# Kernel tuning notes

Hardware: AMD Instinct MI355X
Metric: run time of the kernel (lower is better)

The kernel has to match this reference:

```python
import jax, jax.numpy as jnp
import numpy as np

B, N = 4, 2048
P = N * (N - 1) // 2  # number of upper-triangular pairs
CUTOFF = 5.0
BOX_SCALE = 20.0  # spread points so the 5.0 cutoff gives a sparse graph


def setup_inputs() -> dict:
    key = jax.random.key(0)
    x = jax.random.normal(key, (B, N, 3), dtype=jnp.float32) * BOX_SCALE
    return {"x": x}


def reference(x):
    b, n = x.shape[0], x.shape[1]
    p = n * (n - 1) // 2
    rows, cols = jnp.triu_indices(n, k=1)          # each [P]
    idx0 = jnp.stack([rows, cols], axis=0)          # [2, P]
    # pairwise difference via gather (matches index_select + view in torch)
    diff = x[:, rows, :] - x[:, cols, :]            # [B, P, 3]
    dist = jnp.sqrt(jnp.sum(diff * diff, axis=-1))  # [B, P]
    mask = (dist <= CUTOFF).ravel()                 # [B*P]
    # compaction: valid flat indices first, padded with -1 (jit-static size)
    flat_idx = jnp.nonzero(mask, size=b * p, fill_value=-1)[0]  # [B*P]
    valid = flat_idx >= 0
    safe = jnp.where(valid, flat_idx, 0)
    idx1 = safe // p                                # batch index of each edge
    idx2 = safe % p                                 # pair index of each edge
    out = idx0[:, idx2] + idx1[None, :] * n         # [2, B*P]
    out = jnp.where(valid[None, :], out, -1)        # pad invalid edges with -1
    return out.astype(jnp.int64)
```

## Files before the change

kernel.cpp:

```cpp
#include <hip/hip_runtime.h>
#include <stdint.h>


namespace {
constexpr int kB = 4;
constexpr int kN = 2048;
constexpr int kP = kN * (kN - 1) / 2;
constexpr long long kTotal = (long long)kB * kP;
constexpr float kCut2 = 25.0f;
constexpr int kCap = 128;
constexpr int kNCBlk = 4096;
constexpr int kTile = 256;
constexpr int kNT = kN / kTile;
constexpr int kTPairs = kNT * (kNT + 1) / 2;
constexpr int kJS = 4;
constexpr int kSliceJ = kTile / kJS;
constexpr int kNF = kB * kTPairs * kJS;
constexpr int kFillBlk = 2048;
constexpr int kGrid1 = kNF + kFillBlk;
constexpr int kFillN4 = (int)(2 * kTotal / 4);
constexpr int kFillPerBlk = 2048;
}

__device__ __forceinline__ void decode_pair(int p, int& i, int& j) {
  float t = sqrtf((float)(16769025 - 8 * p));
  int ii = (int)((4095.0f - t) * 0.5f);
  ii = ii < 0 ? 0 : (ii > kN - 2 ? kN - 2 : ii);
  while (ii > 0 && (ii * (4095 - ii)) / 2 > p) --ii;
  while (ii < kN - 2 && ((ii + 1) * (4094 - ii)) / 2 <= p) ++ii;
  i = ii;
  j = ii + 1 + (p - (ii * (4095 - ii)) / 2);
}

__device__ __forceinline__ bool pair_test(const float* __restrict__ x, int b, int p,
                                          int& gi, int& gj) {
  int i, j;
  decode_pair(p, i, j);
  const float* xb = x + (size_t)b * kN * 3;
  float dx = xb[3 * i + 0] - xb[3 * j + 0];
  float dy = xb[3 * i + 1] - xb[3 * j + 1];
  float dz = xb[3 * i + 2] - xb[3 * j + 2];
  gi = b * kN + i;
  gj = b * kN + j;
  return dx * dx + dy * dy + dz * dz <= kCut2;
}

__global__ __launch_bounds__(256) void fill_find_kernel(
    const float* __restrict__ x, uint32_t* __restrict__ counts,
    int2* __restrict__ stash, int* __restrict__ out) {
  const int t = threadIdx.x;
  const int bid = blockIdx.x;

  if (bid >= kNF) {
    const int4 m1 = make_int4(-1, -1, -1, -1);
    int4* o = (int4*)out;
    const int base = (bid - kNF) * kFillPerBlk;
#pragma unroll
    for (int s = 0; s < 8; ++s) {
      const int idx = base + s * 256 + t;
      if (idx < kFillN4) o[idx] = m1;
    }
    return;
  }

  __shared__ float4 sp[kSliceJ];

  const int b = bid / (kTPairs * kJS);
  const int rem = bid - b * (kTPairs * kJS);
  const int u = rem / kJS;
  const int js = rem - u * kJS;
  int ti = 0, rowlen = kNT, acc = 0;
  while (acc + rowlen <= u) { acc += rowlen; --rowlen; ++ti; }
  const int tj = ti + (u - acc);

  const float3* __restrict__ xb3 = (const float3*)(x + (size_t)b * kN * 3);
  const int jbase = tj * kTile + js * kSliceJ;
  if (t < kSliceJ) {
    const float3 pj = xb3[jbase + t];
    sp[t] = make_float4(pj.x, pj.y, pj.z, 0.0f);
  }
  const int i = ti * kTile + t;
  const float3 pi = xb3[i];
  __syncthreads();

  const int gib = b << 11;
  const uint32_t Ci = (uint32_t)((i * (4095 - i)) >> 1);
  const int cbb = b << 10;
  const bool diag = (ti == tj);
  const int jrel0 = js * kSliceJ;

  auto emit = [&](uint32_t m, int jb0) {
    do {
      const int k = __ffs(m) - 1;
      m &= m - 1;
      const int j = jbase + jb0 + k;
      const uint32_t pf = Ci + (uint32_t)(j - i - 1);
      const int cb = cbb + (int)(pf >> 11);
      const uint32_t slot = atomicAdd(&counts[cb], 1u);
      if (slot < (uint32_t)kCap)
        stash[(size_t)cb * kCap + slot] = make_int2(gib + i, gib + j);
    } while (m);
  };

#pragma unroll
  for (int jb = 0; jb < kSliceJ; jb += 8) {
    uint32_t m = 0;
#pragma unroll
    for (int k = 0; k < 8; ++k) {
      const float4 c = sp[jb + k];
      const float dx = pi.x - c.x;
      const float dy = pi.y - c.y;
      const float dz = pi.z - c.z;
      const bool hit = (dx * dx + dy * dy + dz * dz <= kCut2) &&
                       (!diag || (jrel0 + jb + k) > t);
      m |= (uint32_t)hit << k;
    }
    if (m) emit(m, jb);
  }
}

__global__ __launch_bounds__(256) void scatter_kernel(
    const float* __restrict__ x, const uint32_t* __restrict__ counts,
    const int2* __restrict__ stash, int* __restrict__ out) {
  const int bid = blockIdx.x;
  const int t = threadIdx.x;

  const uint32_t cnt = counts[bid];
  if (cnt == 0) return;

  const uint4* c4 = (const uint4*)counts;
  uint32_t part = 0;
#pragma unroll
  for (int q = 0; q < 4; ++q) {
    uint4 v = c4[t * 4 + q];
    int i0 = t * 16 + q * 4;
    part += (i0 + 0 < bid) ? v.x : 0u;
    part += (i0 + 1 < bid) ? v.y : 0u;
    part += (i0 + 2 < bid) ? v.z : 0u;
    part += (i0 + 3 < bid) ? v.w : 0u;
  }
  for (int o = 32; o > 0; o >>= 1) part += __shfl_down(part, o, 64);
  __shared__ uint32_t wred[4];
  if ((t & 63) == 0) wred[t >> 6] = part;
  __syncthreads();
  if (t == 0) wred[0] = wred[0] + wred[1] + wred[2] + wred[3];
  __syncthreads();
  const uint32_t off = wred[0];

  if (cnt <= (uint32_t)kCap) {
    __shared__ int2 ebuf[kCap];
    __shared__ uint32_t pfb[kCap];
    for (uint32_t e = t; e < cnt; e += 256) {
      int2 v = stash[(size_t)bid * kCap + e];
      ebuf[e] = v;
      int i = v.x & 2047, j = v.y & 2047;
      pfb[e] = (uint32_t)((i * (4095 - i)) / 2 + (j - i - 1));
    }
    __syncthreads();
    for (uint32_t e = t; e < cnt; e += 256) {
      uint32_t mypf = pfb[e];
      uint32_t rank = 0;
      for (uint32_t f = 0; f < cnt; ++f) rank += (pfb[f] < mypf) ? 1u : 0u;
      out[off + rank] = ebuf[e].x;
      out[(size_t)kTotal + off + rank] = ebuf[e].y;
    }
    return;
  }

  const int wave = t >> 6, lane = t & 63;
  const int b = bid >> 10;
  const int p0 = (bid & 1023) << 11;
  __shared__ uint32_t slot[32];
  unsigned long long masks[8];
  int gi[8], gj[8];
  bool fl[8];
#pragma unroll
  for (int k = 0; k < 8; ++k) {
    int p = p0 + k * 256 + t;
    fl[k] = (p < kP) && pair_test(x, b, p, gi[k], gj[k]);
    masks[k] = __ballot(fl[k]);
    if (lane == 0) slot[k * 4 + wave] = (uint32_t)__popcll(masks[k]);
  }
  __syncthreads();
  if (t == 0) {
    uint32_t run = 0;
    for (int s = 0; s < 32; ++s) {
      uint32_t c = slot[s];
      slot[s] = run;
      run += c;
    }
  }
  __syncthreads();
#pragma unroll
  for (int k = 0; k < 8; ++k) {
    if (fl[k]) {
      uint32_t pos = off + slot[k * 4 + wave] +
                     (uint32_t)__popcll(masks[k] & ((1ULL << lane) - 1ULL));
      out[pos] = gi[k];
      out[(size_t)kTotal + pos] = gj[k];
    }
  }
}

extern "C" void kernel_launch(void* const* d_in, const int* in_sizes, int n_in,
                              void* d_out, int out_size, void* d_ws, size_t ws_size,
                              hipStream_t stream) {
  const float* x = (const float*)d_in[0];
  int* out = (int*)d_out;
  uint32_t* counts = (uint32_t*)d_ws;
  int2* stash = (int2*)(counts + 4096);

  (void)hipMemsetAsync(counts, 0, kNCBlk * sizeof(uint32_t), stream);
  hipLaunchKernelGGL(fill_find_kernel, dim3(kGrid1), dim3(256), 0, stream, x,
                     counts, stash, out);
  hipLaunchKernelGGL(scatter_kernel, dim3(kNCBlk), dim3(256), 0, stream, x, counts,
                     stash, out);
}
```

Baseline: 31.67 us.

## Move -1 padding fill into output-chunk compose kernel, skipping rewrite of written slots

The -1 fill of the whole output no longer runs as extra blocks inside the find kernel. A second kernel now owns output chunks, and each chunk block writes both the edges and the padding. Blocks whose chunk lies past the total edge count only write -1, while chunks holding edges scan the prefix offsets and write any edges that fall inside their span. The goal is to stop writing -1 into slots that later get edge values, removing double writes and the store-ordering dependency. The cost is serial per-thread rank and recompute loops in the few edge-holding chunks, which could be slow if edges concentrate in a few blocks.

```diff
diff --git a/kernel.cpp b/kernel.cpp
--- a/kernel.cpp
+++ b/kernel.cpp
@@ -16,10 +16,8 @@
 constexpr int kJS = 4;
 constexpr int kSliceJ = kTile / kJS;
 constexpr int kNF = kB * kTPairs * kJS;
-constexpr int kFillBlk = 2048;
-constexpr int kGrid1 = kNF + kFillBlk;
-constexpr int kFillN4 = (int)(2 * kTotal / 4);
-constexpr int kFillPerBlk = 2048;
+constexpr int kChunk = 4096;
+constexpr int kGrid2 = (int)(kTotal / kChunk);
 }
 
 __device__ __forceinline__ void decode_pair(int p, int& i, int& j) {
@@ -45,25 +43,14 @@
   return dx * dx + dy * dy + dz * dz <= kCut2;
 }
 
-__global__ __launch_bounds__(256) void fill_find_kernel(
+__global__ __launch_bounds__(256) void find_kernel(
     const float* __restrict__ x, uint32_t* __restrict__ counts,
-    int2* __restrict__ stash, int* __restrict__ out) {
+    uint32_t* __restrict__ total, int2* __restrict__ stash) {
   const int t = threadIdx.x;
   const int bid = blockIdx.x;
 
-  if (bid >= kNF) {
-    const int4 m1 = make_int4(-1, -1, -1, -1);
-    int4* o = (int4*)out;
-    const int base = (bid - kNF) * kFillPerBlk;
-#pragma unroll
-    for (int s = 0; s < 8; ++s) {
-      const int idx = base + s * 256 + t;
-      if (idx < kFillN4) o[idx] = m1;
-    }
-    return;
-  }
-
   __shared__ float4 sp[kSliceJ];
+  __shared__ uint32_t blkEdges;
 
   const int b = bid / (kTPairs * kJS);
   const int rem = bid - b * (kTPairs * kJS);
@@ -79,6 +66,7 @@
     const float3 pj = xb3[jbase + t];
     sp[t] = make_float4(pj.x, pj.y, pj.z, 0.0f);
   }
+  if (t == 0) blkEdges = 0;
   const int i = ti * kTile + t;
   const float3 pi = xb3[i];
   __syncthreads();
@@ -99,6 +87,7 @@
       const uint32_t slot = atomicAdd(&counts[cb], 1u);
       if (slot < (uint32_t)kCap)
         stash[(size_t)cb * kCap + slot] = make_int2(gib + i, gib + j);
+      atomicAdd(&blkEdges, 1u);
     } while (m);
   };
 
@@ -117,87 +106,132 @@
     }
     if (m) emit(m, jb);
   }
-}
-
-__global__ __launch_bounds__(256) void scatter_kernel(
+
+  __syncthreads();
+  if (t == 0 && blkEdges) atomicAdd(&total[bid & 7], blkEdges);
+}
+
+__global__ __launch_bounds__(256) void fill_compose_kernel(
     const float* __restrict__ x, const uint32_t* __restrict__ counts,
-    const int2* __restrict__ stash, int* __restrict__ out) {
+    const uint32_t* __restrict__ total, const int2* __restrict__ stash,
+    int* __restrict__ out) {
+  const int t = threadIdx.x;
+  const int wave = t >> 6, lane = t & 63;
   const int bid = blockIdx.x;
-  const int t = threadIdx.x;
-
-  const uint32_t cnt = counts[bid];
-  if (cnt == 0) return;
-
-  const uint4* c4 = (const uint4*)counts;
-  uint32_t part = 0;
-#pragma unroll
-  for (int q = 0; q < 4; ++q) {
-    uint4 v = c4[t * 4 + q];
-    int i0 = t * 16 + q * 4;
-    part += (i0 + 0 < bid) ? v.x : 0u;
-    part += (i0 + 1 < bid) ? v.y : 0u;
-    part += (i0 + 2 < bid) ? v.z : 0u;
-    part += (i0 + 3 < bid) ? v.w : 0u;
-  }
-  for (int o = 32; o > 0; o >>= 1) part += __shfl_down(part, o, 64);
+  const int base = bid * kChunk;
+
+  uint32_t T;
+  {
+    const uint4* t4 = (const uint4*)total;
+    uint4 a = t4[0], bb = t4[1];
+    T = a.x + a.y + a.z + a.w + bb.x + bb.y + bb.z + bb.w;
+  }
+
+  int4* o0 = (int4*)out + (base >> 2);
+  int4* o1 = (int4*)(out + kTotal) + (base >> 2);
+
+  if ((uint32_t)base >= T) {
+    const int4 m1 = make_int4(-1, -1, -1, -1);
+#pragma unroll
+    for (int s = 0; s < 4; ++s) {
+      o0[t + s * 256] = m1;
+      o1[t + s * 256] = m1;
+    }
+    return;
+  }
+
+  __shared__ uint32_t offs[kNCBlk];
   __shared__ uint32_t wred[4];
-  if ((t & 63) == 0) wred[t >> 6] = part;
+  {
+    uint32_t c[16];
+    const uint4* c4 = (const uint4*)counts;
+    uint32_t tsum = 0;
+#pragma unroll
+    for (int q = 0; q < 4; ++q) {
+      uint4 v = c4[t * 4 + q];
+      c[q * 4 + 0] = v.x; c[q * 4 + 1] = v.y;
+      c[q * 4 + 2] = v.z; c[q * 4 + 3] = v.w;
+      tsum += v.x + v.y + v.z + v.w;
+    }
+    uint32_t run = tsum;
+    for (int o = 1; o < 64; o <<= 1) {
+      uint32_t u = __shfl_up(run, o, 64);
+      if (lane >= o) run += u;
+    }
+    if (lane == 63) wred[wave] = run;
+    __syncthreads();
+    uint32_t wb = 0;
+    for (int w = 0; w < 4; ++w)
+      if (w < wave) wb += wred[w];
+    uint32_t excl = wb + run - tsum;
+#pragma unroll
+    for (int q = 0; q < 16; ++q) {
+      offs[t * 16 + q] = excl;
+      excl += c[q];
+    }
+  }
   __syncthreads();
-  if (t == 0) wred[0] = wred[0] + wred[1] + wred[2] + wred[3];
-  __syncthreads();
-  const uint32_t off = wred[0];
-
-  if (cnt <= (uint32_t)kCap) {
-    __shared__ int2 ebuf[kCap];
-    __shared__ uint32_t pfb[kCap];
-    for (uint32_t e = t; e < cnt; e += 256) {
-      int2 v = stash[(size_t)bid * kCap + e];
-      ebuf[e] = v;
-      int i = v.x & 2047, j = v.y & 2047;
-      pfb[e] = (uint32_t)((i * (4095 - i)) / 2 + (j - i - 1));
-    }
-    __syncthreads();
-    for (uint32_t e = t; e < cnt; e += 256) {
-      uint32_t mypf = pfb[e];
-      uint32_t rank = 0;
-      for (uint32_t f = 0; f < cnt; ++f) rank += (pfb[f] < mypf) ? 1u : 0u;
-      out[off + rank] = ebuf[e].x;
-      out[(size_t)kTotal + off + rank] = ebuf[e].y;
-    }
-    return;
-  }
-
-  const int wave = t >> 6, lane = t & 63;
-  const int b = bid >> 10;
-  const int p0 = (bid & 1023) << 11;
-  __shared__ uint32_t slot[32];
-  unsigned long long masks[8];
-  int gi[8], gj[8];
-  bool fl[8];
-#pragma unroll
-  for (int k = 0; k < 8; ++k) {
-    int p = p0 + k * 256 + t;
-    fl[k] = (p < kP) && pair_test(x, b, p, gi[k], gj[k]);
-    masks[k] = __ballot(fl[k]);
-    if (lane == 0) slot[k * 4 + wave] = (uint32_t)__popcll(masks[k]);
-  }
-  __syncthreads();
-  if (t == 0) {
-    uint32_t run = 0;
-    for (int s = 0; s < 32; ++s) {
-      uint32_t c = slot[s];
-      slot[s] = run;
-      run += c;
-    }
-  }
-  __syncthreads();
-#pragma unroll
-  for (int k = 0; k < 8; ++k) {
-    if (fl[k]) {
-      uint32_t pos = off + slot[k * 4 + wave] +
-                     (uint32_t)__popcll(masks[k] & ((1ULL << lane) - 1ULL));
-      out[pos] = gi[k];
-      out[(size_t)kTotal + pos] = gj[k];
+
+  const uint32_t spanEnd = (uint32_t)base + (uint32_t)kChunk;
+
+  for (int cb = t; cb < kNCBlk; cb += 256) {
+    const uint32_t o = offs[cb];
+    if (o >= spanEnd) break;
+    const uint32_t cnt = counts[cb];
+    if (cnt == 0 || o + cnt <= (uint32_t)base) continue;
+
+    if (cnt <= (uint32_t)kCap) {
+      for (uint32_t f = 0; f < cnt; ++f) {
+        const int2 vf = stash[(size_t)cb * kCap + f];
+        const int fi = vf.x & 2047, fj = vf.y & 2047;
+        const uint32_t pff = (uint32_t)((fi * (4095 - fi)) / 2 + (fj - fi - 1));
+        uint32_t rank = 0;
+        for (uint32_t g = 0; g < cnt; ++g) {
+          const int2 vg = stash[(size_t)cb * kCap + g];
+          const int gi2 = vg.x & 2047, gj2 = vg.y & 2047;
+          const uint32_t pfg =
+              (uint32_t)((gi2 * (4095 - gi2)) / 2 + (gj2 - gi2 - 1));
+          rank += (pfg < pff) ? 1u : 0u;
+        }
+        const uint32_t pos = o + rank;
+        if (pos >= (uint32_t)base && pos < spanEnd) {
+          out[pos] = vf.x;
+          out[(size_t)kTotal + pos] = vf.y;
+        }
+      }
+    } else {
+      const int b_ = cb >> 10;
+      const int p0 = (cb & 1023) << 11;
+      uint32_t seen = 0;
+      for (int p = p0; p < p0 + 2048 && p < kP; ++p) {
+        int gi_, gj_;
+        if (pair_test(x, b_, p, gi_, gj_)) {
+          const uint32_t pos = o + seen;
+          if (pos >= (uint32_t)base && pos < spanEnd) {
+            out[pos] = gi_;
+            out[(size_t)kTotal + pos] = gj_;
+          }
+          ++seen;
+        }
+      }
+    }
+  }
+
+  {
+    const int4 m1 = make_int4(-1, -1, -1, -1);
+#pragma unroll
+    for (int r = 0; r < 2; ++r) {
+      int* __restrict__ row = out + (size_t)r * kTotal;
+#pragma unroll
+      for (int s = 0; s < 4; ++s) {
+        const int f = base + ((s * 256 + t) << 2);
+        if ((uint32_t)f >= T) {
+          *(int4*)(row + f) = m1;
+        } else if ((uint32_t)f + 4u > T) {
+          for (int e = 0; e < 4; ++e)
+            if ((uint32_t)(f + e) >= T) row[f + e] = -1;
+        }
+      }
     }
   }
 }
@@ -208,11 +242,12 @@
   const float* x = (const float*)d_in[0];
   int* out = (int*)d_out;
   uint32_t* counts = (uint32_t*)d_ws;
-  int2* stash = (int2*)(counts + 4096);
-
-  (void)hipMemsetAsync(counts, 0, kNCBlk * sizeof(uint32_t), stream);
-  hipLaunchKernelGGL(fill_find_kernel, dim3(kGrid1), dim3(256), 0, stream, x,
-                     counts, stash, out);
-  hipLaunchKernelGGL(scatter_kernel, dim3(kNCBlk), dim3(256), 0, stream, x, counts,
-                     stash, out);
-}
+  uint32_t* total = counts + kNCBlk;
+  int2* stash = (int2*)(counts + kNCBlk + 8);
+
+  (void)hipMemsetAsync(counts, 0, (kNCBlk + 8) * sizeof(uint32_t), stream);
+  hipLaunchKernelGGL(find_kernel, dim3(kNF), dim3(256), 0, stream, x, counts,
+                     total, stash);
+  hipLaunchKernelGGL(fill_compose_kernel, dim3(kGrid2), dim3(256), 0, stream, x,
+                     counts, total, stash, out);
+}
```

After: 116.9 us. +268.9%, slower.

## Move -1 padding fill into scatter kernel and skip the valid-edge prefix

Applied to the files above, without the earlier changes.

The -1 fill of the output moves out of the find kernel and into the scatter kernel, and now sets the row and column halves separately. To support this, the find kernel counts edges per block and accumulates a global edge total into eight atomic counters. The fill blocks read that total and write -1 only at positions at or beyond it. This avoids writing -1 over slots the scatter later overwrites and separates the find and fill work. In exchange it adds shared and global atomics to the find kernel. The large fill now shares a launch with scatter instead of overlapping the find phase.

```diff
diff --git a/kernel.cpp b/kernel.cpp
--- a/kernel.cpp
+++ b/kernel.cpp
@@ -7,6 +7,7 @@
 constexpr int kN = 2048;
 constexpr int kP = kN * (kN - 1) / 2;
 constexpr long long kTotal = (long long)kB * kP;
+constexpr int kTotInt = (int)kTotal;
 constexpr float kCut2 = 25.0f;
 constexpr int kCap = 128;
 constexpr int kNCBlk = 4096;
@@ -17,9 +18,7 @@
 constexpr int kSliceJ = kTile / kJS;
 constexpr int kNF = kB * kTPairs * kJS;
 constexpr int kFillBlk = 2048;
-constexpr int kGrid1 = kNF + kFillBlk;
-constexpr int kFillN4 = (int)(2 * kTotal / 4);
-constexpr int kFillPerBlk = 2048;
+constexpr int kGrid2 = kFillBlk + kNCBlk;
 }
 
 __device__ __forceinline__ void decode_pair(int p, int& i, int& j) {
@@ -45,25 +44,14 @@
   return dx * dx + dy * dy + dz * dz <= kCut2;
 }
 
-__global__ __launch_bounds__(256) void fill_find_kernel(
+__global__ __launch_bounds__(256) void find_kernel(
     const float* __restrict__ x, uint32_t* __restrict__ counts,
-    int2* __restrict__ stash, int* __restrict__ out) {
+    uint32_t* __restrict__ total, int2* __restrict__ stash) {
   const int t = threadIdx.x;
   const int bid = blockIdx.x;
 
-  if (bid >= kNF) {
-    const int4 m1 = make_int4(-1, -1, -1, -1);
-    int4* o = (int4*)out;
-    const int base = (bid - kNF) * kFillPerBlk;
-#pragma unroll
-    for (int s = 0; s < 8; ++s) {
-      const int idx = base + s * 256 + t;
-      if (idx < kFillN4) o[idx] = m1;
-    }
-    return;
-  }
-
   __shared__ float4 sp[kSliceJ];
+  __shared__ uint32_t blkEdges;
 
   const int b = bid / (kTPairs * kJS);
   const int rem = bid - b * (kTPairs * kJS);
@@ -79,6 +67,7 @@
     const float3 pj = xb3[jbase + t];
     sp[t] = make_float4(pj.x, pj.y, pj.z, 0.0f);
   }
+  if (t == 0) blkEdges = 0;
   const int i = ti * kTile + t;
   const float3 pi = xb3[i];
   __syncthreads();
@@ -90,9 +79,11 @@
   const int jrel0 = js * kSliceJ;
 
   auto emit = [&](uint32_t m, int jb0) {
+    uint32_t n = 0;
     do {
       const int k = __ffs(m) - 1;
       m &= m - 1;
+      ++n;
       const int j = jbase + jb0 + k;
       const uint32_t pf = Ci + (uint32_t)(j - i - 1);
       const int cb = cbb + (int)(pf >> 11);
@@ -100,6 +91,7 @@
       if (slot < (uint32_t)kCap)
         stash[(size_t)cb * kCap + slot] = make_int2(gib + i, gib + j);
     } while (m);
+    atomicAdd(&blkEdges, n);
   };
 
 #pragma unroll
@@ -117,15 +109,49 @@
     }
     if (m) emit(m, jb);
   }
-}
-
-__global__ __launch_bounds__(256) void scatter_kernel(
+
+  __syncthreads();
+  if (t == 0 && blkEdges) atomicAdd(&total[bid & 7], blkEdges);
+}
+
+__global__ __launch_bounds__(256) void fill_scatter_kernel(
     const float* __restrict__ x, const uint32_t* __restrict__ counts,
-    const int2* __restrict__ stash, int* __restrict__ out) {
+    const uint32_t* __restrict__ total, const int2* __restrict__ stash,
+    int* __restrict__ out) {
+  const int t = threadIdx.x;
   const int bid = blockIdx.x;
-  const int t = threadIdx.x;
-
-  const uint32_t cnt = counts[bid];
+
+  if (bid < kFillBlk) {
+    uint32_t T;
+    {
+      const uint4* t4 = (const uint4*)total;
+      const uint4 a = t4[0], b4 = t4[1];
+      T = a.x + a.y + a.z + a.w + b4.x + b4.y + b4.z + b4.w;
+    }
+    const int4 m1 = make_int4(-1, -1, -1, -1);
+    const int base = bid * 4096;
+#pragma unroll
+    for (int s = 0; s < 4; ++s) {
+      const int f = base + ((s * 256 + t) << 2);
+      if (f >= kTotInt) break;
+      if ((uint32_t)f >= T) {
+        *(int4*)(out + f) = m1;
+        *(int4*)(out + kTotal + f) = m1;
+      } else if ((uint32_t)f + 4u > T) {
+        for (int e = 0; e < 4; ++e) {
+          if ((uint32_t)(f + e) >= T) {
+            out[f + e] = -1;
+            out[kTotal + f + e] = -1;
+          }
+        }
+      }
+    }
+    return;
+  }
+
+  const int sbid = bid - kFillBlk;
+
+  const uint32_t cnt = counts[sbid];
   if (cnt == 0) return;
 
   const uint4* c4 = (const uint4*)counts;
@@ -134,10 +160,10 @@
   for (int q = 0; q < 4; ++q) {
     uint4 v = c4[t * 4 + q];
     int i0 = t * 16 + q * 4;
-    part += (i0 + 0 < bid) ? v.x : 0u;
-    part += (i0 + 1 < bid) ? v.y : 0u;
-    part += (i0 + 2 < bid) ? v.z : 0u;
-    part += (i0 + 3 < bid) ? v.w : 0u;
+    part += (i0 + 0 < sbid) ? v.x : 0u;
+    part += (i0 + 1 < sbid) ? v.y : 0u;
+    part += (i0 + 2 < sbid) ? v.z : 0u;
+    part += (i0 + 3 < sbid) ? v.w : 0u;
   }
   for (int o = 32; o > 0; o >>= 1) part += __shfl_down(part, o, 64);
   __shared__ uint32_t wred[4];
@@ -151,7 +177,7 @@
     __shared__ int2 ebuf[kCap];
     __shared__ uint32_t pfb[kCap];
     for (uint32_t e = t; e < cnt; e += 256) {
-      int2 v = stash[(size_t)bid * kCap + e];
+      int2 v = stash[(size_t)sbid * kCap + e];
       ebuf[e] = v;
       int i = v.x & 2047, j = v.y & 2047;
       pfb[e] = (uint32_t)((i * (4095 - i)) / 2 + (j - i - 1));
@@ -168,8 +194,8 @@
   }
 
   const int wave = t >> 6, lane = t & 63;
-  const int b = bid >> 10;
-  const int p0 = (bid & 1023) << 11;
+  const int b = sbid >> 10;
+  const int p0 = (sbid & 1023) << 11;
   __shared__ uint32_t slot[32];
   unsigned long long masks[8];
   int gi[8], gj[8];
@@ -208,11 +234,12 @@
   const float* x = (const float*)d_in[0];
   int* out = (int*)d_out;
   uint32_t* counts = (uint32_t*)d_ws;
-  int2* stash = (int2*)(counts + 4096);
-
-  (void)hipMemsetAsync(counts, 0, kNCBlk * sizeof(uint32_t), stream);
-  hipLaunchKernelGGL(fill_find_kernel, dim3(kGrid1), dim3(256), 0, stream, x,
-                     counts, stash, out);
-  hipLaunchKernelGGL(scatter_kernel, dim3(kNCBlk), dim3(256), 0, stream, x, counts,
-                     stash, out);
-}
+  uint32_t* total = counts + kNCBlk;
+  int2* stash = (int2*)(counts + kNCBlk + 8);
+
+  (void)hipMemsetAsync(counts, 0, (kNCBlk + 8) * sizeof(uint32_t), stream);
+  hipLaunchKernelGGL(find_kernel, dim3(kNF), dim3(256), 0, stream, x, counts,
+                     total, stash);
+  hipLaunchKernelGGL(fill_scatter_kernel, dim3(kGrid2), dim3(256), 0, stream, x,
+                     counts, total, stash, out);
+}
```

New measurement: 40.13 us. 1.27x slower.

## Replace global bucket stash with per-block LDS edge lists and global rank placement

Applied to the files above, without the earlier changes.

The find kernel now collects hits into a shared-memory list per tile block (LDS atomics) and writes them out with a per-block count. This replaces the global atomic counters and bucketed stash, which also removes the memset. A new place kernel gathers every block's hits into LDS, prefix-sums the counts, and ranks each edge against all edges to find its sorted output position. This removes global atomics and the fallback recompute path, but it makes every active block re-read all hit lists and adds a hard cap on the total edge count (kMaxT), which could give wrong output if that cap is exceeded.

```diff
diff --git a/kernel.cpp b/kernel.cpp
--- a/kernel.cpp
+++ b/kernel.cpp
@@ -8,8 +8,6 @@
 constexpr int kP = kN * (kN - 1) / 2;
 constexpr long long kTotal = (long long)kB * kP;
 constexpr float kCut2 = 25.0f;
-constexpr int kCap = 128;
-constexpr int kNCBlk = 4096;
 constexpr int kTile = 256;
 constexpr int kNT = kN / kTile;
 constexpr int kTPairs = kNT * (kNT + 1) / 2;
@@ -20,6 +18,8 @@
 constexpr int kGrid1 = kNF + kFillBlk;
 constexpr int kFillN4 = (int)(2 * kTotal / 4);
 constexpr int kFillPerBlk = 2048;
+constexpr int kCapF = 1024;
+constexpr int kMaxT = 14336;
 }
 
 __device__ __forceinline__ void decode_pair(int p, int& i, int& j) {
@@ -32,22 +32,9 @@
   j = ii + 1 + (p - (ii * (4095 - ii)) / 2);
 }
 
-__device__ __forceinline__ bool pair_test(const float* __restrict__ x, int b, int p,
-                                          int& gi, int& gj) {
-  int i, j;
-  decode_pair(p, i, j);
-  const float* xb = x + (size_t)b * kN * 3;
-  float dx = xb[3 * i + 0] - xb[3 * j + 0];
-  float dy = xb[3 * i + 1] - xb[3 * j + 1];
-  float dz = xb[3 * i + 2] - xb[3 * j + 2];
-  gi = b * kN + i;
-  gj = b * kN + j;
-  return dx * dx + dy * dy + dz * dz <= kCut2;
-}
-
 __global__ __launch_bounds__(256) void fill_find_kernel(
-    const float* __restrict__ x, uint32_t* __restrict__ counts,
-    int2* __restrict__ stash, int* __restrict__ out) {
+    const float* __restrict__ x, uint32_t* __restrict__ count,
+    uint32_t* __restrict__ fpbuf, int* __restrict__ out) {
   const int t = threadIdx.x;
   const int bid = blockIdx.x;
 
@@ -64,6 +51,8 @@
   }
 
   __shared__ float4 sp[kSliceJ];
+  __shared__ uint32_t lfp[kCapF];
+  __shared__ uint32_t lcnt;
 
   const int b = bid / (kTPairs * kJS);
   const int rem = bid - b * (kTPairs * kJS);
@@ -79,13 +68,13 @@
     const float3 pj = xb3[jbase + t];
     sp[t] = make_float4(pj.x, pj.y, pj.z, 0.0f);
   }
+  if (t == 0) lcnt = 0;
   const int i = ti * kTile + t;
   const float3 pi = xb3[i];
   __syncthreads();
 
-  const int gib = b << 11;
   const uint32_t Ci = (uint32_t)((i * (4095 - i)) >> 1);
-  const int cbb = b << 10;
+  const uint32_t bfp = (uint32_t)b * (uint32_t)kP;
   const bool diag = (ti == tj);
   const int jrel0 = js * kSliceJ;
 
@@ -94,11 +83,9 @@
       const int k = __ffs(m) - 1;
       m &= m - 1;
       const int j = jbase + jb0 + k;
-      const uint32_t pf = Ci + (uint32_t)(j - i - 1);
-      const int cb = cbb + (int)(pf >> 11);
-      const uint32_t slot = atomicAdd(&counts[cb], 1u);
-      if (slot < (uint32_t)kCap)
-        stash[(size_t)cb * kCap + slot] = make_int2(gib + i, gib + j);
+      const uint32_t fp = bfp + Ci + (uint32_t)(j - i - 1);
+      const uint32_t slot = atomicAdd(&lcnt, 1u);
+      if (slot < (uint32_t)kCapF) lfp[slot] = fp;
     } while (m);
   };
 
@@ -117,87 +104,81 @@
     }
     if (m) emit(m, jb);
   }
+
+  __syncthreads();
+  uint32_t c = lcnt;
+  if (c > (uint32_t)kCapF) c = (uint32_t)kCapF;
+  for (uint32_t e = t; e < c; e += 256) fpbuf[(size_t)bid * kCapF + e] = lfp[e];
+  if (t == 0) count[bid] = c;
 }
 
-__global__ __launch_bounds__(256) void scatter_kernel(
-    const float* __restrict__ x, const uint32_t* __restrict__ counts,
-    const int2* __restrict__ stash, int* __restrict__ out) {
-  const int bid = blockIdx.x;
+__global__ __launch_bounds__(256) void place_kernel(
+    const uint32_t* __restrict__ count, const uint32_t* __restrict__ fpbuf,
+    int* __restrict__ out) {
   const int t = threadIdx.x;
+  const int wave = t >> 6, lane = t & 63;
+  const int f = blockIdx.x;
 
-  const uint32_t cnt = counts[bid];
-  if (cnt == 0) return;
+  const uint32_t myc = count[f];
+  if (myc == 0) return;
 
-  const uint4* c4 = (const uint4*)counts;
-  uint32_t part = 0;
+  __shared__ uint32_t cnts[kNF];
+  __shared__ uint32_t pref[kNF];
+  __shared__ uint32_t wred[4];
+  __shared__ uint32_t fpl[kMaxT];
+  __shared__ uint32_t Tsh;
+
+  for (int idx = t; idx < kNF; idx += 256) cnts[idx] = count[idx];
+  __syncthreads();
+
+  const int c0 = t * 3;
+  uint32_t l0 = 0, l1 = 0, l2 = 0, s = 0;
+  if (c0 + 0 < kNF) { l0 = cnts[c0 + 0]; s += l0; }
+  if (c0 + 1 < kNF) { l1 = cnts[c0 + 1]; s += l1; }
+  if (c0 + 2 < kNF) { l2 = cnts[c0 + 2]; s += l2; }
+  uint32_t run = s;
+  for (int o = 1; o < 64; o <<= 1) {
+    uint32_t u = __shfl_up(run, o, 64);
+    if (lane >= o) run += u;
+  }
+  if (lane == 63) wred[wave] = run;
+  __syncthreads();
+  uint32_t wb = 0;
+  for (int w = 0; w < wave; ++w) wb += wred[w];
+  uint32_t excl = wb + run - s;
+  if (c0 + 0 < kNF) { pref[c0 + 0] = excl; excl += l0; }
+  if (c0 + 1 < kNF) { pref[c0 + 1] = excl; excl += l1; }
+  if (c0 + 2 < kNF) { pref[c0 + 2] = excl; excl += l2; }
+  if (t == 191) Tsh = excl;
+  __syncthreads();
+  uint32_t T = Tsh;
+  if (T > (uint32_t)kMaxT) T = (uint32_t)kMaxT;
+
 #pragma unroll
-  for (int q = 0; q < 4; ++q) {
-    uint4 v = c4[t * 4 + q];
-    int i0 = t * 16 + q * 4;
-    part += (i0 + 0 < bid) ? v.x : 0u;
-    part += (i0 + 1 < bid) ? v.y : 0u;
-    part += (i0 + 2 < bid) ? v.z : 0u;
-    part += (i0 + 3 < bid) ? v.w : 0u;
-  }
-  for (int o = 32; o > 0; o >>= 1) part += __shfl_down(part, o, 64);
-  __shared__ uint32_t wred[4];
-  if ((t & 63) == 0) wred[t >> 6] = part;
-  __syncthreads();
-  if (t == 0) wred[0] = wred[0] + wred[1] + wred[2] + wred[3];
-  __syncthreads();
-  const uint32_t off = wred[0];
-
-  if (cnt <= (uint32_t)kCap) {
-    __shared__ int2 ebuf[kCap];
-    __shared__ uint32_t pfb[kCap];
-    for (uint32_t e = t; e < cnt; e += 256) {
-      int2 v = stash[(size_t)bid * kCap + e];
-      ebuf[e] = v;
-      int i = v.x & 2047, j = v.y & 2047;
-      pfb[e] = (uint32_t)((i * (4095 - i)) / 2 + (j - i - 1));
-    }
-    __syncthreads();
-    for (uint32_t e = t; e < cnt; e += 256) {
-      uint32_t mypf = pfb[e];
-      uint32_t rank = 0;
-      for (uint32_t f = 0; f < cnt; ++f) rank += (pfb[f] < mypf) ? 1u : 0u;
-      out[off + rank] = ebuf[e].x;
-      out[(size_t)kTotal + off + rank] = ebuf[e].y;
-    }
-    return;
-  }
-
-  const int wave = t >> 6, lane = t & 63;
-  const int b = bid >> 10;
-  const int p0 = (bid & 1023) << 11;
-  __shared__ uint32_t slot[32];
-  unsigned long long masks[8];
-  int gi[8], gj[8];
-  bool fl[8];
-#pragma unroll
-  for (int k = 0; k < 8; ++k) {
-    int p = p0 + k * 256 + t;
-    fl[k] = (p < kP) && pair_test(x, b, p, gi[k], gj[k]);
-    masks[k] = __ballot(fl[k]);
-    if (lane == 0) slot[k * 4 + wave] = (uint32_t)__popcll(masks[k]);
-  }
-  __syncthreads();
-  if (t == 0) {
-    uint32_t run = 0;
-    for (int s = 0; s < 32; ++s) {
-      uint32_t c = slot[s];
-      slot[s] = run;
-      run += c;
+  for (int q = 0; q < 3; ++q) {
+    const int f2 = c0 + q;
+    if (f2 < kNF) {
+      const uint32_t cc = cnts[f2];
+      const uint32_t bs = pref[f2];
+      for (uint32_t k = 0; k < cc; ++k)
+        if (bs + k < (uint32_t)kMaxT) fpl[bs + k] = fpbuf[(size_t)f2 * kCapF + k];
     }
   }
   __syncthreads();
-#pragma unroll
-  for (int k = 0; k < 8; ++k) {
-    if (fl[k]) {
-      uint32_t pos = off + slot[k * 4 + wave] +
-                     (uint32_t)__popcll(masks[k] & ((1ULL << lane) - 1ULL));
-      out[pos] = gi[k];
-      out[(size_t)kTotal + pos] = gj[k];
+
+  for (uint32_t e = (uint32_t)wave; e < myc; e += 4) {
+    const uint32_t fp = fpbuf[(size_t)f * kCapF + e];
+    uint32_t r = 0;
+    for (uint32_t idx = lane; idx < T; idx += 64)
+      r += (fpl[idx] < fp) ? 1u : 0u;
+    for (int o = 32; o > 0; o >>= 1) r += __shfl_xor(r, o, 64);
+    if (lane == 0) {
+      const int b = (int)(fp / (uint32_t)kP);
+      const int pf = (int)(fp - (uint32_t)b * (uint32_t)kP);
+      int i, j;
+      decode_pair(pf, i, j);
+      out[r] = (b << 11) + i;
+      out[(size_t)kTotal + r] = (b << 11) + j;
     }
   }
 }
@@ -207,12 +188,11 @@
                               hipStream_t stream) {
   const float* x = (const float*)d_in[0];
   int* out = (int*)d_out;
-  uint32_t* counts = (uint32_t*)d_ws;
-  int2* stash = (int2*)(counts + 4096);
+  uint32_t* count = (uint32_t*)d_ws;
+  uint32_t* fpbuf = count + kNF;
 
-  (void)hipMemsetAsync(counts, 0, kNCBlk * sizeof(uint32_t), stream);
   hipLaunchKernelGGL(fill_find_kernel, dim3(kGrid1), dim3(256), 0, stream, x,
-                     counts, stash, out);
-  hipLaunchKernelGGL(scatter_kernel, dim3(kNCBlk), dim3(256), 0, stream, x, counts,
-                     stash, out);
+                     count, fpbuf, out);
+  hipLaunchKernelGGL(place_kernel, dim3(kNF), dim3(256), 0, stream, count, fpbuf,
+                     out);
 }
```

Result: slower. 85.59 us (+170.2%).
